# Kernel tuning notes

Measured on AMD Instinct MI355X. Metric: run time of the kernel, lower is better.

The kernel has to match this reference:

```python
import math
import jax, jax.numpy as jnp
import numpy as np

W_BITS = 8
A_BITS = 8
N_HEADS = 16

def fake_quant(x, bits):
    # symmetric per-tensor fake quantization with straight-through estimator
    if bits >= 32:
        return x
    qmax = float(2 ** (bits - 1) - 1)
    scale = jnp.maximum(jnp.max(jnp.abs(x)) / qmax, 1e-8)
    q = jnp.round(x / scale) * scale
    return x + jax.lax.stop_gradient(q - x)

def qlinear(x, W, b):
    # QuantizeLinear: quantize activations (a_bits) and weights (w_bits), then y = x @ W^T + b
    xq = fake_quant(x, A_BITS)
    Wq = fake_quant(W, W_BITS)
    return jnp.einsum('bsd,ed->bse', xq, Wq) + b

def setup_inputs() -> dict:
    key = jax.random.key(0)
    B, S, D = 2, 2048, 1024
    ks = jax.random.split(key, 6)
    inp = {
        'hidden_states': jax.random.normal(ks[0], (B, S, D), dtype=jnp.float32),
        'attention_mask': jnp.ones((B, S), dtype=jnp.float32),
        'Wq': 0.02 * jax.random.normal(ks[1], (D, D), dtype=jnp.float32),
        'bq': jnp.zeros((D,), dtype=jnp.float32),
        'Wk': 0.02 * jax.random.normal(ks[2], (D, D), dtype=jnp.float32),
        'bk': jnp.zeros((D,), dtype=jnp.float32),
        'Wv': 0.02 * jax.random.normal(ks[3], (D, D), dtype=jnp.float32),
        'bv': jnp.zeros((D,), dtype=jnp.float32),
        'Wo': 0.02 * jax.random.normal(ks[4], (D, D), dtype=jnp.float32),
        'bo': jnp.zeros((D,), dtype=jnp.float32),
    }
    return inp

def reference(hidden_states, attention_mask, Wq, bq, Wk, bk, Wv, bv, Wo, bo):
    B, S, D = hidden_states.shape
    H = N_HEADS
    hd = D // H

    q = qlinear(hidden_states, Wq, bq).reshape(B, S, H, hd)
    k = qlinear(hidden_states, Wk, bk).reshape(B, S, H, hd)
    v = qlinear(hidden_states, Wv, bv).reshape(B, S, H, hd)

    # scores: [B, H, Sq, Sk]
    scores = jnp.einsum('bqhd,bkhd->bhqk', q, k) / math.sqrt(hd)
    mask_bias = (1.0 - attention_mask)[:, None, None, :] * -10000.0
    scores = scores + mask_bias
    probs = jax.nn.softmax(scores, axis=-1)

    attn = jnp.einsum('bhqk,bkhd->bqhd', probs, v).reshape(B, S, D)
    return qlinear(attn, Wo, bo)
```

## Files before the change

### kernel.cpp

```cpp
#include <hip/hip_runtime.h>
#include <cstddef>
#include <cstdint>

constexpr int Bb = 2, Ss = 2048, Dd = 1024, Hh = 16, HD = 64;
constexpr int Mm = Bb * Ss;

typedef int v4i __attribute__((ext_vector_type(4)));
typedef __bf16 bf16x8 __attribute__((ext_vector_type(8)));
typedef __bf16 bf16x2 __attribute__((ext_vector_type(2)));
typedef float f32x16 __attribute__((ext_vector_type(16)));

#define QPOSTMUL 0.18033688f
#define MASKBIAS -14426.950408f

__device__ __forceinline__ float qscale(float amax) {
    return fmaxf(amax / 127.0f, 1e-8f);
}

__device__ __forceinline__ unsigned short bf16rtn(float x) {
    __bf16 b = (__bf16)x;
    return __builtin_bit_cast(unsigned short, b);
}

__device__ __forceinline__ unsigned pack_bf16x2(float a, float b) {
    unsigned ua = __float_as_uint(a), ub = __float_as_uint(b);
    unsigned ha = (ua + 0x7fffu + ((ua >> 16) & 1u)) >> 16;
    unsigned hb = (ub + 0x7fffu + ((ub >> 16) & 1u)) & 0xffff0000u;
    return ha | hb;
}

__global__ void amax_all(const float4* __restrict__ hidden,
                         const float4* __restrict__ w0, const float4* __restrict__ w1,
                         const float4* __restrict__ w2, const float4* __restrict__ w3,
                         unsigned* __restrict__ slots) {
    const float4* src; int n4, slot, bx, nb;
    if (blockIdx.x < 448) { src = hidden; n4 = Mm * Dd / 4; slot = 0; bx = blockIdx.x; nb = 448; }
    else {
        int w = (blockIdx.x - 448) >> 4; bx = (blockIdx.x - 448) & 15; nb = 16;
        src = w == 0 ? w0 : w == 1 ? w1 : w == 2 ? w2 : w3;
        n4 = Dd * Dd / 4; slot = 1 + w;
    }
    float m = 0.f;
    for (int i = bx * blockDim.x + threadIdx.x; i < n4; i += nb * blockDim.x) {
        float4 v = src[i];
        m = fmaxf(m, fmaxf(fmaxf(fabsf(v.x), fabsf(v.y)), fmaxf(fabsf(v.z), fabsf(v.w))));
    }
    #pragma unroll
    for (int off = 32; off > 0; off >>= 1) m = fmaxf(m, __shfl_down(m, off, 64));
    __shared__ float sm[4];
    int lane = threadIdx.x & 63, wid = threadIdx.x >> 6;
    if (lane == 0) sm[wid] = m;
    __syncthreads();
    if (threadIdx.x == 0) {
        float mm = fmaxf(fmaxf(sm[0], sm[1]), fmaxf(sm[2], sm[3]));
        atomicMax(slots + slot, __float_as_uint(mm));
    }
}

__global__ void quant_all(const float* __restrict__ hidden,
                          const float* __restrict__ w0, const float* __restrict__ w1,
                          const float* __restrict__ w2, const float* __restrict__ w3,
                          const float* __restrict__ amax,
                          char* __restrict__ hq8, char* __restrict__ Wall8) {
    const float* x; char* y; int n4, slot, bx, nb;
    if (blockIdx.x < 1024) { x = hidden; y = hq8; n4 = Mm * Dd / 4; slot = 0; bx = blockIdx.x; nb = 1024; }
    else {
        int w = (blockIdx.x - 1024) >> 5; bx = (blockIdx.x - 1024) & 31; nb = 32;
        x = w == 0 ? w0 : w == 1 ? w1 : w == 2 ? w2 : w3;
        y = Wall8 + ((size_t)w << 20);
        n4 = Dd * Dd / 4; slot = 1 + w;
    }
    float s = qscale(amax[slot]);
    const float4* x4 = (const float4*)x;
    char4* y4 = (char4*)y;
    for (int i = bx * blockDim.x + threadIdx.x; i < n4; i += nb * blockDim.x) {
        float4 v = x4[i];
        char4 q;
        q.x = (char)(int)rintf(v.x / s);
        q.y = (char)(int)rintf(v.y / s);
        q.z = (char)(int)rintf(v.z / s);
        q.w = (char)(int)rintf(v.w / s);
        y4[i] = q;
    }
}

__global__ void quant_a(const float* __restrict__ x, char* __restrict__ y,
                        const float* __restrict__ amax, int n4) {
    float s = qscale(amax[0]);
    int stride = gridDim.x * blockDim.x;
    const float4* x4 = (const float4*)x;
    char4* y4 = (char4*)y;
    for (int i = blockIdx.x * blockDim.x + threadIdx.x; i < n4; i += stride) {
        float4 v = x4[i];
        char4 q;
        q.x = (char)(int)rintf(v.x / s);
        q.y = (char)(int)rintf(v.y / s);
        q.z = (char)(int)rintf(v.z / s);
        q.w = (char)(int)rintf(v.w / s);
        y4[i] = q;
    }
}

#define GLOAD_LDS16(g, l) __builtin_amdgcn_global_load_lds( \
    (const __attribute__((address_space(1))) unsigned int*)(g), \
    (__attribute__((address_space(3))) unsigned int*)(l), 16, 0, 0)

__device__ __forceinline__ void gemm128_core(const char* __restrict__ A, const char* __restrict__ Bw,
                                             int bm, int bn, int K, int t,
                                             char* At, char* Bt, v4i acc[4][4]) {
    const int lane = t & 63, w = t >> 6;
    const int wm = (w >> 1) * 64, wn = (w & 1) * 64;
    const int lr = lane & 15, kq = lane >> 4;
    const int rs = w * 16 + (lane >> 2);
    const int cc = lane & 3;

    for (int k0 = 0; k0 < K; k0 += 64) {
        __syncthreads();
        #pragma unroll
        for (int h = 0; h < 2; h++) {
            int r = rs + h * 64;
            int cs = cc ^ ((r >> 1) & 3);
            GLOAD_LDS16(A  + (size_t)(bm + r) * K + k0 + cs * 16, At + r * 64 + cc * 16);
            GLOAD_LDS16(Bw + (size_t)(bn + r) * K + k0 + cs * 16, Bt + r * 64 + cc * 16);
        }
        __syncthreads();

        v4i af[4], bf[4];
        #pragma unroll
        for (int mt = 0; mt < 4; mt++) {
            int row = wm + mt * 16 + lr;
            af[mt] = *(const v4i*)(At + row * 64 + ((kq ^ ((row >> 1) & 3)) << 4));
        }
        #pragma unroll
        for (int nt = 0; nt < 4; nt++) {
            int row = wn + nt * 16 + lr;
            bf[nt] = *(const v4i*)(Bt + row * 64 + ((kq ^ ((row >> 1) & 3)) << 4));
        }
        #pragma unroll
        for (int mt = 0; mt < 4; mt++)
            #pragma unroll
            for (int nt = 0; nt < 4; nt++)
                acc[mt][nt] = __builtin_amdgcn_mfma_i32_16x16x64_i8(af[mt], bf[nt], acc[mt][nt], 0, 0, 0);
    }
}

__global__ __launch_bounds__(256) void gemm_qkv(const char* __restrict__ A,
                                                const char* __restrict__ Wall8,
                                                const float* __restrict__ bq,
                                                const float* __restrict__ bk,
                                                const float* __restrict__ bv,
                                                const float* __restrict__ amax,
                                                unsigned short* __restrict__ qb16,
                                                unsigned short* __restrict__ kb16,
                                                unsigned short* __restrict__ vt16) {
    __shared__ alignas(16) char pool[34816];
    char* At = pool;
    char* Bt = pool + 8192;
    unsigned short (*Tt)[136] = (unsigned short(*)[136])pool;

    const int t = threadIdx.x, lane = t & 63, w = t >> 6;
    const int mat = blockIdx.x >> 3;
    const int bn = (blockIdx.x & 7) * 128, bm = blockIdx.y * 128;
    const int wm = (w >> 1) * 64, wn = (w & 1) * 64;
    const int lr = lane & 15, kq = lane >> 4;

    const v4i vzero = {0, 0, 0, 0};
    v4i acc[4][4];
    #pragma unroll
    for (int mt = 0; mt < 4; mt++)
        #pragma unroll
        for (int nt = 0; nt < 4; nt++) acc[mt][nt] = vzero;

    const char* Bw = Wall8 + ((size_t)mat << 20);
    gemm128_core(A, Bw, bm, bn, Dd, t, At, Bt, acc);

    const float* bias = mat == 0 ? bq : mat == 1 ? bk : bv;
    float sc = qscale(amax[0]) * qscale(amax[1 + mat]);
    float pm = (mat == 0) ? QPOSTMUL : 1.0f;

    __syncthreads();

    if (mat != 2) {
        #pragma unroll
        for (int nt = 0; nt < 4; nt++) {
            int n_l = wn + nt * 16 + lr;
            float bv_ = bias[bn + n_l];
            #pragma unroll
            for (int mt = 0; mt < 4; mt++) {
                int m_l = wm + mt * 16 + kq * 4;
                #pragma unroll
                for (int rg = 0; rg < 4; rg++)
                    Tt[m_l + rg][n_l] = bf16rtn(((float)acc[mt][nt][rg] * sc + bv_) * pm);
            }
        }
    } else {
        #pragma unroll
        for (int nt = 0; nt < 4; nt++) {
            int n_l = wn + nt * 16 + lr;
            float bv_ = bias[bn + n_l];
            #pragma unroll
            for (int mt = 0; mt < 4; mt++) {
                int m_l = wm + mt * 16 + kq * 4;
                ushort4 hv;
                hv.x = bf16rtn((float)acc[mt][nt][0] * sc + bv_);
                hv.y = bf16rtn((float)acc[mt][nt][1] * sc + bv_);
                hv.z = bf16rtn((float)acc[mt][nt][2] * sc + bv_);
                hv.w = bf16rtn((float)acc[mt][nt][3] * sc + bv_);
                *(ushort4*)&Tt[n_l][m_l] = hv;
            }
        }
    }
    __syncthreads();

    {
        int row = t >> 1, half = t & 1;
        unsigned short* dst;
        if (mat != 2) {
            dst = (mat == 0 ? qb16 : kb16) + (size_t)(bm + row) * Dd + bn + half * 64;
        } else {
            int n = bn + row;
            int e = n & 63, hc = n >> 6;
            int b_ = bm >> 11, s_ = (bm & 2047) + half * 64;
            dst = vt16 + (((size_t)(b_ * Hh + hc) * 64 + e) * Ss) + s_;
        }
        const unsigned short* srcl = &Tt[row][half * 64];
        #pragma unroll
        for (int c = 0; c < 8; c++)
            *(int4*)(dst + c * 8) = *(const int4*)(srcl + c * 8);
    }
}

__global__ __launch_bounds__(256) void gemm_o(const char* __restrict__ A,
                                              const char* __restrict__ Bw,
                                              const float* __restrict__ bias,
                                              const float* __restrict__ amaxA,
                                              const float* __restrict__ amaxB,
                                              float* __restrict__ C) {
    __shared__ alignas(16) char At[128 * 64];
    __shared__ alignas(16) char Bt[64 * 64];
    const int t = threadIdx.x, lane = t & 63, w = t >> 6;
    const int bn = blockIdx.x * 64, bm = blockIdx.y * 128;
    const int wm = (w >> 1) * 64, wn = (w & 1) * 32;
    const int lr = lane & 15, kq = lane >> 4;
    const int rs = t >> 2, cc = t & 3;
    const int cs = cc ^ ((rs >> 1) & 3);
    const int rs2 = rs + 64, cs2 = cc ^ ((rs2 >> 1) & 3);

    const v4i vzero = {0, 0, 0, 0};
    v4i acc[4][2];
    #pragma unroll
    for (int mt = 0; mt < 4; mt++) { acc[mt][0] = vzero; acc[mt][1] = vzero; }

    for (int k0 = 0; k0 < Dd; k0 += 64) {
        __syncthreads();
        GLOAD_LDS16(A  + (size_t)(bm + rs)  * Dd + k0 + cs  * 16, At + rs  * 64 + cc * 16);
        GLOAD_LDS16(A  + (size_t)(bm + rs2) * Dd + k0 + cs2 * 16, At + rs2 * 64 + cc * 16);
        GLOAD_LDS16(Bw + (size_t)(bn + rs)  * Dd + k0 + cs  * 16, Bt + rs  * 64 + cc * 16);
        __syncthreads();

        v4i af[4], bf[2];
        #pragma unroll
        for (int mt = 0; mt < 4; mt++) {
            int row = wm + mt * 16 + lr;
            af[mt] = *(const v4i*)(At + row * 64 + ((kq ^ ((row >> 1) & 3)) << 4));
        }
        #pragma unroll
        for (int nt = 0; nt < 2; nt++) {
            int row = wn + nt * 16 + lr;
            bf[nt] = *(const v4i*)(Bt + row * 64 + ((kq ^ ((row >> 1) & 3)) << 4));
        }
        #pragma unroll
        for (int mt = 0; mt < 4; mt++)
            #pragma unroll
            for (int nt = 0; nt < 2; nt++)
                acc[mt][nt] = __builtin_amdgcn_mfma_i32_16x16x64_i8(af[mt], bf[nt], acc[mt][nt], 0, 0, 0);
    }

    float sc = qscale(amaxA[0]) * qscale(amaxB[0]);
    #pragma unroll
    for (int nt = 0; nt < 2; nt++) {
        int n = bn + wn + nt * 16 + lr;
        float bv_ = bias[n];
        #pragma unroll
        for (int mt = 0; mt < 4; mt++)
            #pragma unroll
            for (int rg = 0; rg < 4; rg++) {
                int m = bm + wm + mt * 16 + kq * 4 + rg;
                C[(size_t)m * Dd + n] = (float)acc[mt][nt][rg] * sc + bv_;
            }
    }
}

__global__ __launch_bounds__(256) void attn_mfma(
    const unsigned short* __restrict__ qb16, const unsigned short* __restrict__ kb16,
    const unsigned short* __restrict__ vt16,
    const float* __restrict__ mask, float* __restrict__ Ob, unsigned* __restrict__ amax_out) {
    __shared__ alignas(16) unsigned short KsHi[64][72], VsHi[64][72];
    __shared__ alignas(16) unsigned PwU[4][32][36];
    __shared__ float mbias[64];
    __shared__ float wred[4];

    const int t = threadIdx.x, lane = t & 63, wq = t >> 6;
    const int ln31 = lane & 31, h5 = lane >> 5;
    const int b = blockIdx.z, h = blockIdx.y, q0 = blockIdx.x * 128;

    bf16x8 qf[4];
    {
        int qrow = q0 + wq * 32 + ln31;
        const unsigned short* qb_ = qb16 + ((size_t)(b * Ss + qrow)) * Dd + h * 64 + h5 * 8;
        #pragma unroll
        for (int c = 0; c < 4; c++) qf[c] = *(const bf16x8*)(qb_ + c * 16);
    }

    const int srow = t >> 2, cp = (t & 3) * 2;
    const int rho = (srow >> 1) + (srow & 1) * 32;
    int4 pk0, pk1, pv0, pv1; float pmask = 1.f;
    auto prefetch = [&](int k0) {
        const unsigned short* gk = kb16 + ((size_t)(b * Ss + k0 + srow)) * Dd + h * 64 + cp * 8;
        const unsigned short* gv = vt16 + (((size_t)(b * Hh + h) * 64 + srow)) * Ss + k0 + cp * 8;
        pk0 = *(const int4*)gk; pk1 = *(const int4*)(gk + 8);
        pv0 = *(const int4*)gv; pv1 = *(const int4*)(gv + 8);
        if (t < 64) pmask = mask[b * Ss + k0 + t];
    };

    f32x16 o0 = 0.f, o1 = 0.f;
    float lp[16];
    #pragma unroll
    for (int r = 0; r < 16; r++) lp[r] = 0.f;

    prefetch(0);
    for (int k0 = 0; k0 < Ss; k0 += 64) {
        __syncthreads();
        *(int4*)&KsHi[rho][cp * 8]      = pk0;
        *(int4*)&KsHi[rho][cp * 8 + 8]  = pk1;
        *(int4*)&VsHi[srow][cp * 8]     = pv0;
        *(int4*)&VsHi[srow][cp * 8 + 8] = pv1;
        if (t < 64) mbias[t] = (1.0f - pmask) * MASKBIAS;
        __syncthreads();
        if (k0 + 64 < Ss) prefetch(k0 + 64);

        f32x16 sc0 = 0.f, sc1 = 0.f;
        #pragma unroll
        for (int c = 0; c < 4; c++) {
            bf16x8 kh0 = *(const bf16x8*)&KsHi[ln31][c * 16 + h5 * 8];
            bf16x8 kh1 = *(const bf16x8*)&KsHi[32 + ln31][c * 16 + h5 * 8];
            sc0 = __builtin_amdgcn_mfma_f32_32x32x16_bf16(qf[c], kh0, sc0, 0, 0, 0);
            sc1 = __builtin_amdgcn_mfma_f32_32x32x16_bf16(qf[c], kh1, sc1, 0, 0, 0);
        }

        float mb0 = mbias[2 * ln31], mb1 = mbias[2 * ln31 + 1];
        #pragma unroll
        for (int r = 0; r < 16; r++) {
            float p0 = __builtin_amdgcn_exp2f(sc0[r] + mb0);
            float p1 = __builtin_amdgcn_exp2f(sc1[r] + mb1);
            lp[r] += p0 + p1;
            int row = (r & 3) + 8 * (r >> 2) + 4 * h5;
            PwU[wq][row][ln31] = pack_bf16x2(p0, p1);
        }

        #pragma unroll
        for (int c = 0; c < 4; c++) {
            bf16x8 pf = *(const bf16x8*)((const unsigned short*)&PwU[wq][ln31][0] + c * 16 + h5 * 8);
            bf16x8 vh0 = *(const bf16x8*)&VsHi[ln31][c * 16 + h5 * 8];
            bf16x8 vh1 = *(const bf16x8*)&VsHi[32 + ln31][c * 16 + h5 * 8];
            o0 = __builtin_amdgcn_mfma_f32_32x32x16_bf16(pf, vh0, o0, 0, 0, 0);
            o1 = __builtin_amdgcn_mfma_f32_32x32x16_bf16(pf, vh1, o1, 0, 0, 0);
        }
    }

    float lmax = 0.f;
    #pragma unroll
    for (int r = 0; r < 16; r++) {
        float l = lp[r];
        #pragma unroll
        for (int off = 1; off < 32; off <<= 1) l += __shfl_xor(l, off, 32);
        float inv = 1.0f / l;
        int row = q0 + wq * 32 + (r & 3) + 8 * (r >> 2) + 4 * h5;
        size_t ro = ((size_t)(b * Ss + row)) * Dd + h * 64;
        float v0 = o0[r] * inv, v1 = o1[r] * inv;
        Ob[ro + ln31] = v0;
        Ob[ro + 32 + ln31] = v1;
        lmax = fmaxf(lmax, fmaxf(fabsf(v0), fabsf(v1)));
    }
    #pragma unroll
    for (int off = 32; off > 0; off >>= 1) lmax = fmaxf(lmax, __shfl_xor(lmax, off, 64));
    if (lane == 0) wred[wq] = lmax;
    __syncthreads();
    if (t == 0) {
        float m = fmaxf(fmaxf(wred[0], wred[1]), fmaxf(wred[2], wred[3]));
        atomicMax(amax_out, __float_as_uint(m));
    }
}

extern "C" void kernel_launch(void* const* d_in, const int* in_sizes, int n_in,
                              void* d_out, int out_size, void* d_ws, size_t ws_size,
                              hipStream_t stream) {
    const float* hidden = (const float*)d_in[0];
    const float* mask   = (const float*)d_in[1];
    const float* Wq = (const float*)d_in[2];
    const float* bq = (const float*)d_in[3];
    const float* Wk = (const float*)d_in[4];
    const float* bk = (const float*)d_in[5];
    const float* Wv = (const float*)d_in[6];
    const float* bv = (const float*)d_in[7];
    const float* Wo = (const float*)d_in[8];
    const float* bo = (const float*)d_in[9];
    float* out = (float*)d_out;

    char* ws = (char*)d_ws;
    float* scal = (float*)ws;
    size_t off = 1024;
    const size_t szH8 = (size_t)Mm * Dd;
    const size_t szHb = (size_t)Mm * Dd * sizeof(unsigned short);
    const size_t szHf = (size_t)Mm * Dd * sizeof(float);
    char* hq8   = ws + off; off += szH8;
    char* Wall8 = ws + off; off += 4u << 20;
    char* aq8   = ws + off; off += szH8;
    unsigned short* qb16 = (unsigned short*)(ws + off); off += szHb;
    unsigned short* kb16 = (unsigned short*)(ws + off); off += szHb;
    unsigned short* vt16 = (unsigned short*)(ws + off); off += szHb;
    float* ab = (float*)(ws + off); off += szHf;

    hipMemsetAsync(scal, 0, 64, stream);

    amax_all<<<512, 256, 0, stream>>>((const float4*)hidden, (const float4*)Wq,
                                      (const float4*)Wk, (const float4*)Wv, (const float4*)Wo,
                                      (unsigned*)scal);
    quant_all<<<1152, 256, 0, stream>>>(hidden, Wq, Wk, Wv, Wo, scal, hq8, Wall8);

    gemm_qkv<<<dim3(24, 32), 256, 0, stream>>>(hq8, Wall8, bq, bk, bv, scal,
                                               qb16, kb16, vt16);

    attn_mfma<<<dim3(Ss / 128, Hh, Bb), 256, 0, stream>>>(qb16, kb16, vt16,
                                                          mask, ab, (unsigned*)(scal + 5));

    quant_a<<<1024, 256, 0, stream>>>(ab, aq8, scal + 5, Mm * Dd / 4);

    gemm_o<<<dim3(16, 32), 256, 0, stream>>>(aq8, Wall8 + (3u << 20), bo,
                                             scal + 5, scal + 4, out);
}
```

Baseline: 232.7 us.

## Split attention key range across two wave groups per block and merge partials

The attention kernel now launches 512 threads per block. Two groups of four waves each process half of the key sequence with separate shared K/V tiles. The partial outputs and row sums are merged through shared memory, which reuses the K/V buffers, before normalisation and the amax reduction. This doubles the waves in flight per query tile to hide latency, at the cost of more shared memory and registers per block and an extra merge step. The change also adds s_setprio around the MFMA sections and replaces the manual bf16 rounding with the compiler's bf16 conversion.

```diff
diff --git a/kernel.cpp b/kernel.cpp
--- a/kernel.cpp
+++ b/kernel.cpp
@@ -23,10 +23,10 @@
 }
 
 __device__ __forceinline__ unsigned pack_bf16x2(float a, float b) {
-    unsigned ua = __float_as_uint(a), ub = __float_as_uint(b);
-    unsigned ha = (ua + 0x7fffu + ((ua >> 16) & 1u)) >> 16;
-    unsigned hb = (ub + 0x7fffu + ((ub >> 16) & 1u)) & 0xffff0000u;
-    return ha | hb;
+    bf16x2 h;
+    h[0] = (__bf16)a;
+    h[1] = (__bf16)b;
+    return __builtin_bit_cast(unsigned, h);
 }
 
 __global__ void amax_all(const float4* __restrict__ hidden,
@@ -291,28 +291,32 @@
     }
 }
 
-__global__ __launch_bounds__(256) void attn_mfma(
+__global__ __launch_bounds__(512) void attn_mfma(
     const unsigned short* __restrict__ qb16, const unsigned short* __restrict__ kb16,
     const unsigned short* __restrict__ vt16,
     const float* __restrict__ mask, float* __restrict__ Ob, unsigned* __restrict__ amax_out) {
-    __shared__ alignas(16) unsigned short KsHi[64][72], VsHi[64][72];
-    __shared__ alignas(16) unsigned PwU[4][32][36];
-    __shared__ float mbias[64];
+    __shared__ alignas(16) char apool[36864];
+    unsigned short (*Ks)[64][72] = (unsigned short(*)[64][72])apool;
+    unsigned short (*Vs)[64][72] = (unsigned short(*)[64][72])(apool + 18432);
+    __shared__ alignas(16) unsigned PwU[8][32][36];
+    __shared__ float mbias[2][64];
     __shared__ float wred[4];
 
     const int t = threadIdx.x, lane = t & 63, wq = t >> 6;
+    const int g = wq >> 2, wq4 = wq & 3, tg = t & 255;
     const int ln31 = lane & 31, h5 = lane >> 5;
     const int b = blockIdx.z, h = blockIdx.y, q0 = blockIdx.x * 128;
+    const int kbase = g << 10;
 
     bf16x8 qf[4];
     {
-        int qrow = q0 + wq * 32 + ln31;
+        int qrow = q0 + wq4 * 32 + ln31;
         const unsigned short* qb_ = qb16 + ((size_t)(b * Ss + qrow)) * Dd + h * 64 + h5 * 8;
         #pragma unroll
         for (int c = 0; c < 4; c++) qf[c] = *(const bf16x8*)(qb_ + c * 16);
     }
 
-    const int srow = t >> 2, cp = (t & 3) * 2;
+    const int srow = tg >> 2, cp = (tg & 3) * 2;
     const int rho = (srow >> 1) + (srow & 1) * 32;
     int4 pk0, pk1, pv0, pv1; float pmask = 1.f;
     auto prefetch = [&](int k0) {
@@ -320,7 +324,7 @@
         const unsigned short* gv = vt16 + (((size_t)(b * Hh + h) * 64 + srow)) * Ss + k0 + cp * 8;
         pk0 = *(const int4*)gk; pk1 = *(const int4*)(gk + 8);
         pv0 = *(const int4*)gv; pv1 = *(const int4*)(gv + 8);
-        if (t < 64) pmask = mask[b * Ss + k0 + t];
+        if (tg < 64) pmask = mask[b * Ss + k0 + tg];
     };
 
     f32x16 o0 = 0.f, o1 = 0.f;
@@ -328,27 +332,29 @@
     #pragma unroll
     for (int r = 0; r < 16; r++) lp[r] = 0.f;
 
-    prefetch(0);
-    for (int k0 = 0; k0 < Ss; k0 += 64) {
-        __syncthreads();
-        *(int4*)&KsHi[rho][cp * 8]      = pk0;
-        *(int4*)&KsHi[rho][cp * 8 + 8]  = pk1;
-        *(int4*)&VsHi[srow][cp * 8]     = pv0;
-        *(int4*)&VsHi[srow][cp * 8 + 8] = pv1;
-        if (t < 64) mbias[t] = (1.0f - pmask) * MASKBIAS;
-        __syncthreads();
-        if (k0 + 64 < Ss) prefetch(k0 + 64);
+    prefetch(kbase);
+    for (int k0 = kbase; k0 < kbase + Ss / 2; k0 += 64) {
+        __syncthreads();
+        *(int4*)&Ks[g][rho][cp * 8]      = pk0;
+        *(int4*)&Ks[g][rho][cp * 8 + 8]  = pk1;
+        *(int4*)&Vs[g][srow][cp * 8]     = pv0;
+        *(int4*)&Vs[g][srow][cp * 8 + 8] = pv1;
+        if (tg < 64) mbias[g][tg] = (1.0f - pmask) * MASKBIAS;
+        __syncthreads();
+        if (k0 + 64 < kbase + Ss / 2) prefetch(k0 + 64);
 
         f32x16 sc0 = 0.f, sc1 = 0.f;
+        __builtin_amdgcn_s_setprio(1);
         #pragma unroll
         for (int c = 0; c < 4; c++) {
-            bf16x8 kh0 = *(const bf16x8*)&KsHi[ln31][c * 16 + h5 * 8];
-            bf16x8 kh1 = *(const bf16x8*)&KsHi[32 + ln31][c * 16 + h5 * 8];
+            bf16x8 kh0 = *(const bf16x8*)&Ks[g][ln31][c * 16 + h5 * 8];
+            bf16x8 kh1 = *(const bf16x8*)&Ks[g][32 + ln31][c * 16 + h5 * 8];
             sc0 = __builtin_amdgcn_mfma_f32_32x32x16_bf16(qf[c], kh0, sc0, 0, 0, 0);
             sc1 = __builtin_amdgcn_mfma_f32_32x32x16_bf16(qf[c], kh1, sc1, 0, 0, 0);
         }
-
-        float mb0 = mbias[2 * ln31], mb1 = mbias[2 * ln31 + 1];
+        __builtin_amdgcn_s_setprio(0);
+
+        float mb0 = mbias[g][2 * ln31], mb1 = mbias[g][2 * ln31 + 1];
         #pragma unroll
         for (int r = 0; r < 16; r++) {
             float p0 = __builtin_amdgcn_exp2f(sc0[r] + mb0);
@@ -358,33 +364,56 @@
             PwU[wq][row][ln31] = pack_bf16x2(p0, p1);
         }
 
+        __builtin_amdgcn_s_setprio(1);
         #pragma unroll
         for (int c = 0; c < 4; c++) {
             bf16x8 pf = *(const bf16x8*)((const unsigned short*)&PwU[wq][ln31][0] + c * 16 + h5 * 8);
-            bf16x8 vh0 = *(const bf16x8*)&VsHi[ln31][c * 16 + h5 * 8];
-            bf16x8 vh1 = *(const bf16x8*)&VsHi[32 + ln31][c * 16 + h5 * 8];
+            bf16x8 vh0 = *(const bf16x8*)&Vs[g][ln31][c * 16 + h5 * 8];
+            bf16x8 vh1 = *(const bf16x8*)&Vs[g][32 + ln31][c * 16 + h5 * 8];
             o0 = __builtin_amdgcn_mfma_f32_32x32x16_bf16(pf, vh0, o0, 0, 0, 0);
             o1 = __builtin_amdgcn_mfma_f32_32x32x16_bf16(pf, vh1, o1, 0, 0, 0);
         }
-    }
-
-    float lmax = 0.f;
-    #pragma unroll
-    for (int r = 0; r < 16; r++) {
-        float l = lp[r];
-        #pragma unroll
-        for (int off = 1; off < 32; off <<= 1) l += __shfl_xor(l, off, 32);
-        float inv = 1.0f / l;
-        int row = q0 + wq * 32 + (r & 3) + 8 * (r >> 2) + 4 * h5;
-        size_t ro = ((size_t)(b * Ss + row)) * Dd + h * 64;
-        float v0 = o0[r] * inv, v1 = o1[r] * inv;
-        Ob[ro + ln31] = v0;
-        Ob[ro + 32 + ln31] = v1;
-        lmax = fmaxf(lmax, fmaxf(fabsf(v0), fabsf(v1)));
-    }
-    #pragma unroll
-    for (int off = 32; off > 0; off >>= 1) lmax = fmaxf(lmax, __shfl_xor(lmax, off, 64));
-    if (lane == 0) wred[wq] = lmax;
+        __builtin_amdgcn_s_setprio(0);
+    }
+
+    __syncthreads();
+    float (*Osh)[65] = (float(*)[65])apool;
+    float* Lsh = (float*)(apool + 33280);
+
+    if (g == 1) {
+        #pragma unroll
+        for (int r = 0; r < 16; r++) {
+            float l = lp[r];
+            #pragma unroll
+            for (int off = 1; off < 32; off <<= 1) l += __shfl_xor(l, off, 32);
+            int rl = wq4 * 32 + (r & 3) + 8 * (r >> 2) + 4 * h5;
+            Osh[rl][ln31]      = o0[r];
+            Osh[rl][32 + ln31] = o1[r];
+            if (ln31 == 0) Lsh[rl] = l;
+        }
+    }
+    __syncthreads();
+    if (g == 0) {
+        float lmax = 0.f;
+        #pragma unroll
+        for (int r = 0; r < 16; r++) {
+            float l = lp[r];
+            #pragma unroll
+            for (int off = 1; off < 32; off <<= 1) l += __shfl_xor(l, off, 32);
+            int rl = wq4 * 32 + (r & 3) + 8 * (r >> 2) + 4 * h5;
+            float inv = 1.0f / (l + Lsh[rl]);
+            int row = q0 + rl;
+            size_t ro = ((size_t)(b * Ss + row)) * Dd + h * 64;
+            float v0 = (o0[r] + Osh[rl][ln31]) * inv;
+            float v1 = (o1[r] + Osh[rl][32 + ln31]) * inv;
+            Ob[ro + ln31]      = v0;
+            Ob[ro + 32 + ln31] = v1;
+            lmax = fmaxf(lmax, fmaxf(fabsf(v0), fabsf(v1)));
+        }
+        #pragma unroll
+        for (int off = 32; off > 0; off >>= 1) lmax = fmaxf(lmax, __shfl_xor(lmax, off, 64));
+        if (lane == 0) wred[wq4] = lmax;
+    }
     __syncthreads();
     if (t == 0) {
         float m = fmaxf(fmaxf(wred[0], wred[1]), fmaxf(wred[2], wred[3]));
@@ -431,7 +460,7 @@
     gemm_qkv<<<dim3(24, 32), 256, 0, stream>>>(hq8, Wall8, bq, bk, bv, scal,
                                                qb16, kb16, vt16);
 
-    attn_mfma<<<dim3(Ss / 128, Hh, Bb), 256, 0, stream>>>(qb16, kb16, vt16,
+    attn_mfma<<<dim3(Ss / 128, Hh, Bb), 512, 0, stream>>>(qb16, kb16, vt16,
                                                           mask, ab, (unsigned*)(scal + 5));
 
     quant_a<<<1024, 256, 0, stream>>>(ab, aq8, scal + 5, Mm * Dd / 4);
```

After: 232.5 us. No clear change (-0.1%).
